# Optimization experiments

Measured on AMD Instinct MI355X. Metric: run time of the kernel, lower is better.

Reference implementation:

```python
import jax, jax.numpy as jnp
import numpy as np

B, S, I, H = 2, 400, 80, 128
F = 2 * H            # bidirectional feature dim
N = S + 1            # zero row prepended -> pairwise grid size
MAX_SEG = 50
NCLS = 50


def prelu(x, a):
    return jnp.where(x >= 0, x, a * x)


def lstm_dir(x, Wi, Wh, b, reverse=False):
    # x: (B, S, I); torch gate order: i, f, g, o
    if reverse:
        x = x[:, ::-1]
    Hd = Wh.shape[1]

    def step(carry, xt):
        h, c = carry
        gates = xt @ Wi.T + h @ Wh.T + b
        i_, f_, g_, o_ = jnp.split(gates, 4, axis=-1)
        c = jax.nn.sigmoid(f_) * c + jax.nn.sigmoid(i_) * jnp.tanh(g_)
        h = jax.nn.sigmoid(o_) * jnp.tanh(c)
        return (h, c), h

    h0 = jnp.zeros((x.shape[0], Hd), x.dtype)
    _, hs = jax.lax.scan(step, (h0, h0), jnp.swapaxes(x, 0, 1))
    hs = jnp.swapaxes(hs, 0, 1)
    if reverse:
        hs = hs[:, ::-1]
    return hs


def setup_inputs() -> dict:
    key = jax.random.key(0)
    ks = jax.random.split(key, 16)

    def rn(k, shape, s=0.05):
        return jax.random.normal(k, shape, jnp.float32) * s

    inp = {
        "x": jax.random.normal(ks[0], (B, S, I), jnp.float32),
        "lengths": jnp.full((B,), S, jnp.int32),
        "Wi_f": rn(ks[1], (4 * H, I)), "Wh_f": rn(ks[2], (4 * H, H)), "b_f": jnp.zeros((4 * H,), jnp.float32),
        "Wi_b": rn(ks[3], (4 * H, I)), "Wh_b": rn(ks[4], (4 * H, H)), "b_b": jnp.zeros((4 * H,), jnp.float32),
        "a1": jnp.full((1,), 0.25, jnp.float32),
        "W1": rn(ks[5], (100, 3 * F)), "b1": jnp.zeros((100,), jnp.float32),
        "a2": jnp.full((1,), 0.25, jnp.float32),
        "W2": rn(ks[6], (1, 100)), "b2": jnp.zeros((1,), jnp.float32),
        "ac1": jnp.full((1,), 0.25, jnp.float32),
        "Wc1": rn(ks[7], (2 * NCLS, F)), "bc1": jnp.zeros((2 * NCLS,), jnp.float32),
        "ac2": jnp.full((1,), 0.25, jnp.float32),
        "Wc2": rn(ks[8], (NCLS, 2 * NCLS)), "bc2": jnp.zeros((NCLS,), jnp.float32),
        "ab1": jnp.full((1,), 0.25, jnp.float32),
        "Wb1": rn(ks[9], (2 * NCLS, F)), "bb1": jnp.zeros((2 * NCLS,), jnp.float32),
        "ab2": jnp.full((1,), 0.25, jnp.float32),
        "Wb2": rn(ks[10], (2, 2 * NCLS)), "bb2": jnp.zeros((2,), jnp.float32),
    }
    return inp


def compute_scores(x, Wi_f, Wh_f, b_f, Wi_b, Wh_b, b_b, a1, W1, b1, a2, W2, b2):
    rnn_out = jnp.concatenate(
        [lstm_dir(x, Wi_f, Wh_f, b_f, False), lstm_dir(x, Wi_b, Wh_b, b_b, True)], axis=-1
    )  # (B, S, F)
    xp = jnp.concatenate([jnp.zeros((x.shape[0], 1, F), x.dtype), rnn_out], axis=1)  # (B, N, F)
    cum = jnp.cumsum(xp, axis=1)
    # phi[b,i,j] = concat(cum[j]-cum[i], xp[i], xp[j]); PReLU is elementwise with a
    # single shared parameter, and the first Linear is additive across the concat
    # blocks, so we decompose W1 instead of materializing the (B,N,N,3F) tensor.
    W1c, W1d, W1e = W1[:, :F], W1[:, F:2 * F], W1[:, 2 * F:]
    pc = prelu(cum[:, None, :, :] - cum[:, :, None, :], a1)  # (B, N, N, F)
    pxd = prelu(xp, a1) @ W1d.T                              # (B, N, 100)
    pxe = prelu(xp, a1) @ W1e.T                              # (B, N, 100)
    h = jnp.einsum('bijf,kf->bijk', pc, W1c) + pxd[:, :, None, :] + pxe[:, None, :, :] + b1
    scores = (prelu(h, a2) @ W2.T + b2)[..., 0]              # (B, N, N)
    return rnn_out, scores


def segment_search(scores):
    # DP: best[i] = max_{max(0,i-MAX_SEG) <= k < i} best[k] + scores[:, k, i]
    Bn, Nn = scores.shape[0], scores.shape[1]
    ks = jnp.arange(Nn)

    def dp_step(best, i):
        col = jnp.take(scores, i, axis=2)                    # (B, N)
        mask = (ks >= i - MAX_SEG) & (ks < i)
        cand = jnp.where(mask[None, :], best + col, -jnp.inf)
        m = cand.max(axis=1)
        k = cand.argmax(axis=1)
        best = best.at[:, i].set(m)
        return best, k

    best0 = jnp.zeros((Bn, Nn), scores.dtype)
    best, prev_tail = jax.lax.scan(dp_step, best0, jnp.arange(1, Nn))
    prev = jnp.concatenate([jnp.zeros((Bn, 1), jnp.int32),
                            prev_tail.T.astype(jnp.int32)], axis=1)  # (B, N)
    return best, prev


def reference(x, lengths, Wi_f, Wh_f, b_f, Wi_b, Wh_b, b_b, a1, W1, b1, a2, W2, b2,
              ac1, Wc1, bc1, ac2, Wc2, bc2, ab1, Wb1, bb1, ab2, Wb2, bb2):
    rnn_out, scores = compute_scores(x, Wi_f, Wh_f, b_f, Wi_b, Wh_b, b_b,
                                     a1, W1, b1, a2, W2, b2)
    cls_out = prelu(prelu(rnn_out, ac1) @ Wc1.T + bc1, ac2) @ Wc2.T + bc2
    bin_out = prelu(prelu(rnn_out, ab1) @ Wb1.T + bb1, ab2) @ Wb2.T + bb2
    best, prev = segment_search(scores)
    # pred score for the best segmentation ending at `lengths[b]` equals best[b, L]
    pred_scores = best[jnp.arange(scores.shape[0]), lengths]
    return scores, cls_out, bin_out, pred_scores, prev
```

## Files before the change

### kernel.cpp

```cpp
#include <hip/hip_runtime.h>
#include <hip/hip_fp16.h>
#include <math.h>

#define BB 2
#define SS 400
#define II 80
#define HH 128
#define FF 256
#define NN 401
#define G4 512
#define MAXSEG 50
#define NCLS 50
#define KH 100
#define KP 112
#define FRAGF 14336

#define SCORES_OFF 0
#define CLS_OFF    (BB*NN*NN)
#define BIN_OFF    (CLS_OFF + BB*SS*NCLS)
#define PRED_OFF   (BIN_OFF + BB*SS*2)
#define PREV_OFF   (PRED_OFF + BB)

#define WS_GX      0
#define WS_RNN     (WS_GX + 4*SS*G4)
#define WS_CUM     (WS_RNN + BB*SS*FF)
#define WS_PXD     (WS_CUM + BB*NN*FF)
#define WS_PXE     (WS_PXD + BB*NN*KP)
#define WS_PART    (WS_PXE + BB*NN*KP)
#define WS_W2P     (WS_PART + BB*16*FF)
#define WS_B1P     (WS_W2P + KP)
#define WS_WHP     (WS_B1P + KP)
#define WS_WFRAGC  (WS_WHP + 65536)
#define WS_WFRAGD  (WS_WFRAGC + FRAGF)
#define WS_WFRAGE  (WS_WFRAGD + FRAGF)
#define WS_WFRAGHC (WS_WFRAGE + FRAGF)
#define WS_WFRAGHB (WS_WFRAGHC + FRAGF)
#define WS_BC1P    (WS_WFRAGHB + FRAGF)
#define WS_BB1P    (WS_BC1P + KP)

typedef __attribute__((ext_vector_type(8))) short short8;
typedef __attribute__((ext_vector_type(4))) float f32x4;
typedef _Float16 f16x2 __attribute__((ext_vector_type(2)));
typedef _Float16 f16x8 __attribute__((ext_vector_type(8)));

__device__ __forceinline__ float prelu_f(float x, float a) {
    return x >= 0.f ? x : a * x;
}
__device__ __forceinline__ unsigned short f2bf(float x) {
    union { float f; unsigned u; } v; v.f = x;
    unsigned r = v.u + 0x7fffu + ((v.u >> 16) & 1u);
    return (unsigned short)(r >> 16);
}
__device__ __forceinline__ float fast_sigmoid(float x) {
    return 1.f / (1.f + __expf(-x));
}
__device__ __forceinline__ float fast_tanh(float x) {
    return 1.f - 2.f / (1.f + __expf(2.f * x));
}
__device__ __forceinline__ void barrier_lds() {
    asm volatile("s_waitcnt lgkmcnt(0)\ns_barrier" ::: "memory");
}
__device__ __forceinline__ void rec_barrier() {
    __builtin_amdgcn_sched_barrier(0);
    asm volatile("s_waitcnt lgkmcnt(0)");
    __builtin_amdgcn_s_barrier();
    __builtin_amdgcn_sched_barrier(0);
}
__device__ __forceinline__ int fragidx(int k, int f) {
    int kt = k >> 4, l15 = k & 15;
    int ks = f >> 5, quad = (f >> 3) & 3, e = f & 7;
    return ((((kt * 8 + ks) * 4 + quad) * 16) + l15) * 8 + e;
}

#define WPACKS (5 * KP)
#define PREPBLKS (WPACKS + G4)
__global__ void k_lstm_pre(const float* __restrict__ x,
                           const float* __restrict__ Wi_f, const float* __restrict__ b_f,
                           const float* __restrict__ Wi_b, const float* __restrict__ b_b,
                           float* __restrict__ gx,
                           const float* __restrict__ W1, const float* __restrict__ W2,
                           const float* __restrict__ b1,
                           const float* __restrict__ Wh_f, const float* __restrict__ Wh_b,
                           const float* __restrict__ Wc1, const float* __restrict__ Wb1,
                           const float* __restrict__ bc1, const float* __restrict__ bb1,
                           short* __restrict__ wfC, short* __restrict__ wfD,
                           short* __restrict__ wfE, short* __restrict__ wfHC,
                           short* __restrict__ wfHB,
                           float* __restrict__ w2p, float* __restrict__ b1p,
                           float* __restrict__ bc1p, float* __restrict__ bb1p,
                           __half* __restrict__ whp) {
    int blk0 = blockIdx.x;
    int tid = threadIdx.x;
    if (blk0 < WPACKS) {
        int which = blk0 / KP;
        int k = blk0 % KP;
        float w = 0.f;
        short* dst = wfC;
        if (which == 0)      { if (k < KH) w = W1[k * (3 * FF) + tid];          dst = wfC; }
        else if (which == 1) { if (k < KH) w = W1[k * (3 * FF) + FF + tid];     dst = wfD; }
        else if (which == 2) { if (k < KH) w = W1[k * (3 * FF) + 2 * FF + tid]; dst = wfE; }
        else if (which == 3) { if (k < KH) w = Wc1[k * FF + tid];               dst = wfHC; }
        else                 { if (k < KH) w = Wb1[k * FF + tid];               dst = wfHB; }
        dst[fragidx(k, tid)] = (short)f2bf(w);
        if (tid == 0) {
            if (which == 0) {
                w2p[k] = (k < KH) ? W2[k] : 0.f;
                b1p[k] = (k < KH) ? b1[k] : 0.f;
            } else if (which == 3) {
                bc1p[k] = (k < KH) ? bc1[k] : 0.f;
            } else if (which == 4) {
                bb1p[k] = (k < KH) ? bb1[k] : 0.f;
            }
        }
        return;
    }
    if (blk0 < PREPBLKS) {
        int gq = blk0 - WPACKS;
        int gate = gq >> 7;
        int unit = gq & 127;
        int wv = unit >> 4, col = unit & 15;
        int dir = tid >> 7, k = tid & 127;
        int kt = k >> 5, lanehi = (k >> 3) & 3, e = k & 7;
        int lane = lanehi * 16 + col;
        const float* Wh = dir ? Wh_b : Wh_f;
        whp[(size_t)(((((dir * 4 + gate) * 8 + wv) * 4 + kt) * 64) + lane) * 8 + e] =
            (__half)Wh[gq * HH + k];
        return;
    }
    int blk = blk0 - PREPBLKS;
    int t = blk % SS;
    int db = blk / SS;
    int b = db & 1, dir = db >> 1;
    const float* Wi = dir ? Wi_b : Wi_f;
    const float* bias = dir ? b_b : b_f;
    int xt = dir ? (SS - 1 - t) : t;

    __shared__ __align__(16) float xr[II];
    if (tid < II) xr[tid] = x[(b * SS + xt) * II + tid];
    __syncthreads();

    for (int g = tid; g < G4; g += 256) {
        const float* w = Wi + g * II;
        float acc = bias[g];
#pragma unroll
        for (int i = 0; i < II; i += 4) {
            float4 w4 = *(const float4*)(w + i);
            acc += w4.x * xr[i] + w4.y * xr[i + 1] + w4.z * xr[i + 2] + w4.w * xr[i + 3];
        }
        gx[((size_t)(db * SS + t) * HH + (g & 127)) * 4 + (g >> 7)] = acc;
    }
}

__global__ __launch_bounds__(512, 1)
void k_lstm_rec(const _Float16* __restrict__ whf, const float* __restrict__ gxr,
                float* __restrict__ rnn_out) {
    int db = blockIdx.x;
    int b = db & 1, dir = db >> 1;
    int tid = threadIdx.x;
    int wv = tid >> 6;
    int lane = tid & 63;

    f16x8 bf[4][4];
    {
        const f16x8* wp = (const f16x8*)whf;
#pragma unroll
        for (int g = 0; g < 4; ++g)
#pragma unroll
            for (int kt = 0; kt < 4; ++kt)
                bf[g][kt] = wp[((((dir * 4 + g) * 8 + wv) * 4 + kt) * 64) + lane];
    }

    __shared__ __align__(16) __half hsf[2][128];
    for (int i = tid; i < 256; i += 512) (&hsf[0][0])[i] = (__half)0.f;
    __syncthreads();

    float c_state = 0.f;
    const float4* gp4 = (const float4*)gxr + (size_t)(db * SS) * HH
                      + (wv << 4) + (lane & 15);

    float4 g0 = make_float4(0,0,0,0), g1 = g0, g2 = g0, g3 = g0;
    if (lane < 16) {
        g0 = gp4[0 * HH];
        g1 = gp4[1 * HH];
        g2 = gp4[2 * HH];
        g3 = gp4[3 * HH];
    }

    f16x8 a[4];
#pragma unroll
    for (int kt = 0; kt < 4; ++kt) a[kt] = (f16x8)(_Float16)0.f;

    int pb = 0;

#define REC_STEP(IOFF, G) do {                                                 \
        \
        if ((lane & 15) == 0) {                                                \
            _Pragma("unroll")                                                  \
            for (int kt = 0; kt < 4; ++kt)                                     \
                a[kt] = *(const f16x8*)(&hsf[pb][kt * 32 + (lane >> 4) * 8]);  \
        }                                                                      \
        f32x4 acc0 = (f32x4){0.f,0.f,0.f,0.f};                                 \
        f32x4 acc1 = acc0, acc2 = acc0, acc3 = acc0;                           \
        _Pragma("unroll")                                                      \
        for (int kt = 0; kt < 4; ++kt) {                                       \
            acc0 = __builtin_amdgcn_mfma_f32_16x16x32_f16(a[kt], bf[0][kt], acc0, 0, 0, 0); \
            acc1 = __builtin_amdgcn_mfma_f32_16x16x32_f16(a[kt], bf[1][kt], acc1, 0, 0, 0); \
            acc2 = __builtin_amdgcn_mfma_f32_16x16x32_f16(a[kt], bf[2][kt], acc2, 0, 0, 0); \
            acc3 = __builtin_amdgcn_mfma_f32_16x16x32_f16(a[kt], bf[3][kt], acc3, 0, 0, 0); \
        }                                                                      \
        if (lane < 16) {                                                       \
            float gi = acc0[0] + G.x;                                          \
            float gf = acc1[0] + G.y;                                          \
            float gg = acc2[0] + G.z;                                          \
            float go = acc3[0] + G.w;                                          \
            c_state = fast_sigmoid(gf) * c_state + fast_sigmoid(gi) * fast_tanh(gg); \
            float h = fast_sigmoid(go) * fast_tanh(c_state);                   \
            hsf[pb ^ 1][(wv << 4) + lane] = (__half)h;                         \
            int t_ = step + (IOFF);                                            \
            int xt = dir ? (SS - 1 - t_) : t_;                                 \
            rnn_out[(b * SS + xt) * FF + dir * HH + (wv << 4) + lane] = h;     \
                             \
            G = (t_ + 4 < SS) ? gp4[(size_t)(t_ + 4) * HH]                     \
                              : make_float4(0.f, 0.f, 0.f, 0.f);               \
        }                                                                      \
        rec_barrier();                                                         \
        pb ^= 1;                                                               \
    } while (0)

    for (int step = 0; step < SS; step += 4) {
        REC_STEP(0, g0);
        REC_STEP(1, g1);
        REC_STEP(2, g2);
        REC_STEP(3, g3);
    }
#undef REC_STEP
}

#define CHUNK 25
#define NCH 16
__global__ void k_cum_part(const float* __restrict__ rnn, float* __restrict__ part) {
    int blk = blockIdx.x;
    int c = blk % NCH, b = blk / NCH;
    int f = threadIdx.x;
    float s = 0.f;
    for (int r = 0; r < CHUNK; ++r) s += rnn[(b * SS + c * CHUNK + r) * FF + f];
    part[blk * FF + f] = s;
}
__global__ void k_cum_off(float* __restrict__ part) {
    int b = blockIdx.x;
    int f = threadIdx.x;
    float run = 0.f;
    for (int c = 0; c < NCH; ++c) {
        int idx = (b * NCH + c) * FF + f;
        float tmp = part[idx];
        part[idx] = run;
        run += tmp;
    }
}
__global__ void k_cum_write(const float* __restrict__ rnn, const float* __restrict__ part,
                            float* __restrict__ cum) {
    int blk = blockIdx.x;
    int c = blk % NCH, b = blk / NCH;
    int f = threadIdx.x;
    float run = part[blk * FF + f];
    cum[(b * NN + c * CHUNK) * FF + f] = run;
    for (int idx = 1; idx <= CHUNK; ++idx) {
        run += rnn[(b * SS + c * CHUNK + idx - 1) * FF + f];
        cum[(b * NN + c * CHUNK + idx) * FF + f] = run;
    }
}

#define PXBLKS 26
#define HDBLKS 25
#define AP 272
#define UCP 116
__global__ __launch_bounds__(256, 2)
void k_mlp(const float* __restrict__ rnn,
           const float* __restrict__ a1p,
           const float* __restrict__ ac1p, const float* __restrict__ ab1p,
           const short* __restrict__ wfD, const short* __restrict__ wfE,
           const short* __restrict__ wfHC, const short* __restrict__ wfHB,
           const float* __restrict__ bc1p, const float* __restrict__ bb1p,
           const float* __restrict__ ac2p, const float* __restrict__ ab2p,
           const float* __restrict__ Wc2, const float* __restrict__ bc2,
           const float* __restrict__ Wb2, const float* __restrict__ bb2,
           float* __restrict__ pxd, float* __restrict__ pxe,
           float* __restrict__ cls_out, float* __restrict__ bin_out) {
    int blk = blockIdx.x;
    int tid = threadIdx.x;
    bool is_px = (blk < PXBLKS);
    int rowbase = is_px ? blk * 32 : (blk - PXBLKS) * 32;
    int nrows_tot = is_px ? BB * NN : BB * SS;

    __shared__ __align__(16) short dth[2][32][AP];
    __shared__ float ucsh[2][32][UCP];

    {
        int row = tid >> 3;
        int fb = (tid & 7) * 32;
        int rg = rowbase + row;
        float src[32];
        if (is_px) {
            float a1 = a1p[0];
            int b = rg / NN, n = rg % NN;
            bool valid = (rg < nrows_tot) && (n > 0);
            const float* sp = valid ? (rnn + (b * SS + n - 1) * FF + fb) : nullptr;
#pragma unroll
            for (int c4 = 0; c4 < 8; ++c4) {
                float4 v = valid ? *(const float4*)(sp + c4 * 4) : make_float4(0,0,0,0);
                src[c4*4] = v.x; src[c4*4+1] = v.y; src[c4*4+2] = v.z; src[c4*4+3] = v.w;
            }
            union { short8 s; unsigned short u[8]; } h8;
#pragma unroll
            for (int c8 = 0; c8 < 4; ++c8) {
#pragma unroll
                for (int e = 0; e < 8; ++e) h8.u[e] = f2bf(prelu_f(src[c8*8+e], a1));
                *(short8*)(&dth[0][row][fb + c8 * 8]) = h8.s;
            }
        } else {
            float ac1 = ac1p[0], ab1 = ab1p[0];
            bool valid = (rg < nrows_tot);
            const float* sp = valid ? (rnn + rg * FF + fb) : nullptr;
#pragma unroll
            for (int c4 = 0; c4 < 8; ++c4) {
                float4 v = valid ? *(const float4*)(sp + c4 * 4) : make_float4(0,0,0,0);
                src[c4*4] = v.x; src[c4*4+1] = v.y; src[c4*4+2] = v.z; src[c4*4+3] = v.w;
            }
            union { short8 s; unsigned short u[8]; } hc, hb;
#pragma unroll
            for (int c8 = 0; c8 < 4; ++c8) {
#pragma unroll
                for (int e = 0; e < 8; ++e) {
                    hc.u[e] = f2bf(prelu_f(src[c8*8+e], ac1));
                    hb.u[e] = f2bf(prelu_f(src[c8*8+e], ab1));
                }
                *(short8*)(&dth[0][row][fb + c8 * 8]) = hc.s;
                *(short8*)(&dth[1][row][fb + c8 * 8]) = hb.s;
            }
        }
    }
    __syncthreads();

    int lane = tid & 63;
    int wv = tid >> 6;
    int quad = lane >> 4;
    int l15 = lane & 15;
    int kt0 = wv * 2, kt1 = wv * 2 + 1;
    bool has1 = (kt1 < 7);

    const short8* wp0 = (const short8*)(is_px ? wfD : wfHC);
    const short8* wp1 = (const short8*)(is_px ? wfE : wfHB);

    f32x4 acc[2][2][2];
#pragma unroll
    for (int p = 0; p < 2; ++p)
#pragma unroll
        for (int mt = 0; mt < 2; ++mt)
#pragma unroll
            for (int kk = 0; kk < 2; ++kk) acc[p][mt][kk] = (f32x4){0.f,0.f,0.f,0.f};

#pragma unroll
    for (int ks = 0; ks < 8; ++ks) {
        short8 b00 = wp0[((kt0 * 8 + ks) * 4 + quad) * 16 + l15];
        short8 b01 = has1 ? wp0[((kt1 * 8 + ks) * 4 + quad) * 16 + l15] : b00;
        short8 b10 = wp1[((kt0 * 8 + ks) * 4 + quad) * 16 + l15];
        short8 b11 = has1 ? wp1[((kt1 * 8 + ks) * 4 + quad) * 16 + l15] : b10;
#pragma unroll
        for (int mt = 0; mt < 2; ++mt) {
            short8 a0 = *(const short8*)(&dth[0][mt * 16 + l15][ks * 32 + quad * 8]);
            short8 a1v = is_px ? a0
                       : *(const short8*)(&dth[1][mt * 16 + l15][ks * 32 + quad * 8]);
            acc[0][mt][0] = __builtin_amdgcn_mfma_f32_16x16x32_bf16(a0, b00, acc[0][mt][0], 0, 0, 0);
            acc[1][mt][0] = __builtin_amdgcn_mfma_f32_16x16x32_bf16(a1v, b10, acc[1][mt][0], 0, 0, 0);
            if (has1) {
                acc[0][mt][1] = __builtin_amdgcn_mfma_f32_16x16x32_bf16(a0, b01, acc[0][mt][1], 0, 0, 0);
                acc[1][mt][1] = __builtin_amdgcn_mfma_f32_16x16x32_bf16(a1v, b11, acc[1][mt][1], 0, 0, 0);
            }
        }
    }

    int kout0 = kt0 * 16 + l15;
    int kout1 = has1 ? (kt1 * 16 + l15) : 0;

    if (is_px) {
#pragma unroll
        for (int mt = 0; mt < 2; ++mt) {
#pragma unroll
            for (int r = 0; r < 4; ++r) {
                int m = mt * 16 + quad * 4 + r;
                int rg = rowbase + m;
                if (rg < nrows_tot) {
                    pxd[rg * KP + kout0] = acc[0][mt][0][r];
                    pxe[rg * KP + kout0] = acc[1][mt][0][r];
                    if (has1) {
                        pxd[rg * KP + kout1] = acc[0][mt][1][r];
                        pxe[rg * KP + kout1] = acc[1][mt][1][r];
                    }
                }
            }
        }
        return;
    }

    float bc0 = bc1p[kout0], bc1v = bc1p[kout1];
    float bb0 = bb1p[kout0], bb1v = bb1p[kout1];
    float ac2 = ac2p[0], ab2 = ab2p[0];
#pragma unroll
    for (int mt = 0; mt < 2; ++mt) {
#pragma unroll
        for (int r = 0; r < 4; ++r) {
            int m = mt * 16 + quad * 4 + r;
            ucsh[0][m][kout0] = prelu_f(acc[0][mt][0][r] + bc0, ac2);
            ucsh[1][m][kout0] = prelu_f(acc[1][mt][0][r] + bb0, ab2);
            if (has1) {
                ucsh[0][m][kout1] = prelu_f(acc[0][mt][1][r] + bc1v, ac2);
                ucsh[1][m][kout1] = prelu_f(acc[1][mt][1][r] + bb1v, ab2);
            }
        }
    }
    __syncthreads();
    {
        int row = tid >> 3;
        int oc = tid & 7;
        int rg = rowbase + row;
        bool valid = (rg < nrows_tot);
        for (int o = oc; o < NCLS; o += 8) {
            float s = bc2[o];
            const float* w = Wc2 + o * KH;
#pragma unroll 4
            for (int k = 0; k < KH; ++k) s += w[k] * ucsh[0][row][k];
            if (valid) cls_out[rg * NCLS + o] = s;
        }
        if (tid < 64) {
            int row2 = tid >> 1, o = tid & 1;
            int rg2 = rowbase + row2;
            float s = bb2[o];
            const float* w = Wb2 + o * KH;
#pragma unroll 4
            for (int k = 0; k < KH; ++k) s += w[k] * ucsh[1][row2][k];
            if (rg2 < nrows_tot) bin_out[rg2 * 2 + o] = s;
        }
    }
}

#define JT 32
#define JTILES 13
#define NP2 201
__global__ __launch_bounds__(256, 3)
void k_scores(const float* __restrict__ cum,
              const short* __restrict__ wfrag,
              const float* __restrict__ pxd, const float* __restrict__ pxe,
              const float* __restrict__ b1p, const float* __restrict__ w2p,
              const float* __restrict__ b2p,
              const float* __restrict__ a1p, const float* __restrict__ a2p,
              float* __restrict__ scores, float* __restrict__ dpcol) {
    int blk = blockIdx.x;
    int jt = blk % JTILES;
    int ipair = (blk / JTILES) % NP2;
    int b = blk / (JTILES * NP2);
    int tid = threadIdx.x;
    float a1 = a1p[0], a2 = a2p[0];
    int jbase = jt * JT;
    int i0 = ipair * 2;
    int i1 = i0 + 1;
    bool has_i1 = (i1 <= SS);
    int i1c = has_i1 ? i1 : i0;

    __shared__ __align__(16) float cish[2][FF];
    __shared__ __align__(16) short dth[2][JT][AP];
    __shared__ float red[2][4][JT];

    cish[0][tid] = cum[(b * NN + i0) * FF + tid];
    cish[1][tid] = cum[(b * NN + i1c) * FF + tid];
    __syncthreads();

    {
        int row = tid >> 3;
        int fb = (tid & 7) * 32;
        int jg = jbase + row;
        int jc = (jg <= SS) ? jg : SS;
        const float* cj = cum + (b * NN + jc) * FF + fb;
        float4 v[8];
#pragma unroll
        for (int c8 = 0; c8 < 4; ++c8) {
            v[2 * c8] = *(const float4*)(cj + c8 * 8);
            v[2 * c8 + 1] = *(const float4*)(cj + c8 * 8 + 4);
        }
#pragma unroll
        for (int ii = 0; ii < 2; ++ii) {
            const float* cio = &cish[ii][0];
#pragma unroll
            for (int c8 = 0; c8 < 4; ++c8) {
                float dv[8] = { v[2*c8].x, v[2*c8].y, v[2*c8].z, v[2*c8].w,
                                v[2*c8+1].x, v[2*c8+1].y, v[2*c8+1].z, v[2*c8+1].w };
                union { short8 s; unsigned short u[8]; } h8;
#pragma unroll
                for (int e = 0; e < 8; ++e) {
                    float d = prelu_f(dv[e] - cio[fb + c8 * 8 + e], a1);
                    h8.u[e] = f2bf(d);
                }
                *(short8*)(&dth[ii][row][fb + c8 * 8]) = h8.s;
            }
        }
    }
    __syncthreads();

    int lane = tid & 63;
    int wv = tid >> 6;
    int quad = lane >> 4;
    int l15 = lane & 15;
    int kt0 = wv * 2, kt1 = wv * 2 + 1;
    bool has1 = (kt1 < 7);

    const short8* wf = (const short8*)wfrag;
    f32x4 acc[2][2][2];
#pragma unroll
    for (int ii = 0; ii < 2; ++ii)
#pragma unroll
        for (int mt = 0; mt < 2; ++mt)
#pragma unroll
            for (int kk = 0; kk < 2; ++kk) acc[ii][mt][kk] = (f32x4){0.f,0.f,0.f,0.f};

#pragma unroll
    for (int ks = 0; ks < 8; ++ks) {
        short8 b0 = wf[((kt0 * 8 + ks) * 4 + quad) * 16 + l15];
        short8 b1v = has1 ? wf[((kt1 * 8 + ks) * 4 + quad) * 16 + l15] : b0;
#pragma unroll
        for (int ii = 0; ii < 2; ++ii) {
#pragma unroll
            for (int mt = 0; mt < 2; ++mt) {
                short8 a = *(const short8*)(&dth[ii][mt * 16 + l15][ks * 32 + quad * 8]);
                acc[ii][mt][0] = __builtin_amdgcn_mfma_f32_16x16x32_bf16(a, b0, acc[ii][mt][0], 0, 0, 0);
                if (has1)
                    acc[ii][mt][1] = __builtin_amdgcn_mfma_f32_16x16x32_bf16(a, b1v, acc[ii][mt][1], 0, 0, 0);
            }
        }
    }

    int kout0 = kt0 * 16 + l15;
    int kout1 = has1 ? (kt1 * 16 + l15) : 0;
    float bb0 = b1p[kout0], bb1v = b1p[kout1];
    float w20 = w2p[kout0];
    float w21 = has1 ? w2p[kout1] : 0.f;

#pragma unroll
    for (int ii = 0; ii < 2; ++ii) {
        int iv = ii ? i1c : i0;
        float pd0 = pxd[(b * NN + iv) * KP + kout0];
        float pd1 = pxd[(b * NN + iv) * KP + kout1];
#pragma unroll
        for (int mt = 0; mt < 2; ++mt) {
#pragma unroll
            for (int r = 0; r < 4; ++r) {
                int m = mt * 16 + quad * 4 + r;
                int jg = jbase + m;
                int jc = (jg <= SS) ? jg : SS;
                float pe0 = pxe[(b * NN + jc) * KP + kout0];
                float pe1 = pxe[(b * NN + jc) * KP + kout1];
                float h0 = acc[ii][mt][0][r] + pd0 + pe0 + bb0;
                float s = w20 * prelu_f(h0, a2);
                float h1 = acc[ii][mt][1][r] + pd1 + pe1 + bb1v;
                s += w21 * prelu_f(h1, a2);
                s += __shfl_xor(s, 1);
                s += __shfl_xor(s, 2);
                s += __shfl_xor(s, 4);
                s += __shfl_xor(s, 8);
                if (l15 == 0) red[ii][wv][m] = s;
            }
        }
    }
    __syncthreads();
    if (tid < 2 * JT) {
        int ii = tid >> 5;
        int jl = tid & 31;
        int jg = jbase + jl;
        int iv = ii ? i1 : i0;
        if (jg <= SS && (ii == 0 || has_i1)) {
            float tot = red[ii][0][jl] + red[ii][1][jl] + red[ii][2][jl] + red[ii][3][jl] + b2p[0];
            scores[(b * NN + iv) * NN + jg] = tot;
            int d = jg - iv;
            if (d >= 1 && d <= MAXSEG) {
                dpcol[(b * NN + jg) * 64 + (iv & 63)] = tot;
            }
        }
    }
}

__global__ void k_dp(const float* __restrict__ dpcol, const int* __restrict__ lengths,
                     float* __restrict__ predF, float* __restrict__ prevF) {
    int b = blockIdx.x;
    int lane = threadIdx.x;
    int len = lengths[b];
    if (lane == 0) prevF[b * NN] = 0.f;

    float blr = 0.f;
    float predv = 0.f;

#define LO(I) (((I) > MAXSEG) ? ((I) - MAXSEG) : 0)
#define LOADCOL(ii) \
    ( ((ii) <= SS && (((lane - LO(ii)) & 63) < ((ii) - LO(ii)))) \
        ? dpcol[(b * NN + (ii)) * 64 + lane] : 0.f )

    float u0 = LOADCOL(1), u1 = LOADCOL(2), u2 = LOADCOL(3), u3 = LOADCOL(4);
    float u4 = LOADCOL(5), u5 = LOADCOL(6), u6 = LOADCOL(7), u7 = LOADCOL(8);

#define DPP_LVL(CTRL, v, k) do {                                              \
        int vo_i = __builtin_amdgcn_update_dpp(__float_as_int(v),             \
                       __float_as_int(v), (CTRL), 0xF, 0xF, false);           \
        int ko_  = __builtin_amdgcn_update_dpp((k), (k), (CTRL), 0xF, 0xF, false); \
        float vo = __int_as_float(vo_i);                                      \
        bool take = (vo > (v)) || (vo == (v) && ko_ < (k));                   \
        (v) = take ? vo : (v);                                                \
        (k) = take ? ko_ : (k);                                               \
    } while (0)

#define DP_STEP(I, BUF) do {                                                  \
        int lo_ = LO(I);                                                      \
        int cnt_ = (I) - lo_;                                                 \
        int off_ = (lane - lo_) & 63;                                         \
        float v_ = (off_ < cnt_) ? blr + BUF : -INFINITY;                     \
        int k_ = lo_ + off_;                                                  \
        DPP_LVL(0x111, v_, k_);                               \
        DPP_LVL(0x112, v_, k_);                               \
        DPP_LVL(0x114, v_, k_);                               \
        DPP_LVL(0x118, v_, k_);                               \
        DPP_LVL(0x142, v_, k_);                             \
        DPP_LVL(0x143, v_, k_);                             \
        int kb_ = __builtin_amdgcn_readlane(k_, 63);                          \
        float m_ = __int_as_float(                                            \
            __builtin_amdgcn_readlane(__float_as_int(v_), 63));               \
        if (lane == 0) {                                                      \
            prevF[b * NN + (I)] = (float)kb_;                                 \
            if ((I) == len) predv = m_;                                       \
        }                                                                     \
        if (lane == ((I) & 63)) blr = m_;                                     \
    } while (0)

    for (int i = 1; i <= SS; i += 8) {
        DP_STEP(i, u0);     u0 = LOADCOL(i + 8);
        DP_STEP(i + 1, u1); u1 = LOADCOL(i + 9);
        DP_STEP(i + 2, u2); u2 = LOADCOL(i + 10);
        DP_STEP(i + 3, u3); u3 = LOADCOL(i + 11);
        DP_STEP(i + 4, u4); u4 = LOADCOL(i + 12);
        DP_STEP(i + 5, u5); u5 = LOADCOL(i + 13);
        DP_STEP(i + 6, u6); u6 = LOADCOL(i + 14);
        DP_STEP(i + 7, u7); u7 = LOADCOL(i + 15);
    }
#undef DP_STEP
#undef DPP_LVL
#undef LOADCOL
#undef LO
    if (lane == 0) predF[b] = predv;
}

extern "C" void kernel_launch(void* const* d_in, const int* in_sizes, int n_in,
                              void* d_out, int out_size, void* d_ws, size_t ws_size,
                              hipStream_t stream) {
    const float* x    = (const float*)d_in[0];
    const int* lengths= (const int*)d_in[1];
    const float* Wi_f = (const float*)d_in[2];
    const float* Wh_f = (const float*)d_in[3];
    const float* b_f  = (const float*)d_in[4];
    const float* Wi_b = (const float*)d_in[5];
    const float* Wh_b = (const float*)d_in[6];
    const float* b_b  = (const float*)d_in[7];
    const float* a1   = (const float*)d_in[8];
    const float* W1   = (const float*)d_in[9];
    const float* b1   = (const float*)d_in[10];
    const float* a2   = (const float*)d_in[11];
    const float* W2   = (const float*)d_in[12];
    const float* b2   = (const float*)d_in[13];
    const float* ac1  = (const float*)d_in[14];
    const float* Wc1  = (const float*)d_in[15];
    const float* bc1  = (const float*)d_in[16];
    const float* ac2  = (const float*)d_in[17];
    const float* Wc2  = (const float*)d_in[18];
    const float* bc2  = (const float*)d_in[19];
    const float* ab1  = (const float*)d_in[20];
    const float* Wb1  = (const float*)d_in[21];
    const float* bb1  = (const float*)d_in[22];
    const float* ab2  = (const float*)d_in[23];
    const float* Wb2  = (const float*)d_in[24];
    const float* bb2  = (const float*)d_in[25];

    float* out = (float*)d_out;
    float* scores = out + SCORES_OFF;
    float* cls    = out + CLS_OFF;
    float* bin    = out + BIN_OFF;
    float* pred   = out + PRED_OFF;
    float* prev   = out + PREV_OFF;

    float* ws    = (float*)d_ws;
    float* gx    = ws + WS_GX;
    float* dpcol = ws + WS_GX;
    float* rnn   = ws + WS_RNN;
    float* cum   = ws + WS_CUM;
    float* pxd   = ws + WS_PXD;
    float* pxe   = ws + WS_PXE;
    float* part  = ws + WS_PART;
    float* w2p   = ws + WS_W2P;
    float* b1p   = ws + WS_B1P;
    __half* whp  = (__half*)(ws + WS_WHP);
    short* wfC   = (short*)(ws + WS_WFRAGC);
    short* wfD   = (short*)(ws + WS_WFRAGD);
    short* wfE   = (short*)(ws + WS_WFRAGE);
    short* wfHC  = (short*)(ws + WS_WFRAGHC);
    short* wfHB  = (short*)(ws + WS_WFRAGHB);
    float* bc1p  = ws + WS_BC1P;
    float* bb1p  = ws + WS_BB1P;

    k_lstm_pre<<<PREPBLKS + 4 * SS, 256, 0, stream>>>(x, Wi_f, b_f, Wi_b, b_b, gx,
                                                      W1, W2, b1, Wh_f, Wh_b,
                                                      Wc1, Wb1, bc1, bb1,
                                                      wfC, wfD, wfE, wfHC, wfHB,
                                                      w2p, b1p, bc1p, bb1p, whp);
    k_lstm_rec<<<4, 512, 0, stream>>>((const _Float16*)whp, gx, rnn);
    k_cum_part<<<BB * NCH, FF, 0, stream>>>(rnn, part);
    k_cum_off<<<BB, FF, 0, stream>>>(part);
    k_cum_write<<<BB * NCH, FF, 0, stream>>>(rnn, part, cum);
    k_mlp<<<PXBLKS + HDBLKS, 256, 0, stream>>>(rnn, a1, ac1, ab1,
                                               wfD, wfE, wfHC, wfHB,
                                               bc1p, bb1p, ac2, ab2,
                                               Wc2, bc2, Wb2, bb2,
                                               pxd, pxe, cls, bin);
    k_scores<<<BB * NP2 * JTILES, 256, 0, stream>>>(cum, wfC, pxd, pxe, b1p, w2p, b2,
                                                    a1, a2, scores, dpcol);
    k_dp<<<BB, 64, 0, stream>>>(dpcol, lengths, pred, prev);
}
```

Before: 638.1 us.

## Streamline LSTM recurrence step and merge prefix-sum kernels into one

The recurrent step now has every lane load the h fragments from shared memory directly, not just one lane per 16. The MFMA chain is fully unrolled with a zero-initialised first accumulate, and the gate prefetch uses a moving pointer with a peeled final iteration instead of per-step bounds checks. Output stores use an incrementing pointer rather than recomputed indices. The three-kernel chunked cumulative sum is replaced by one serial-scan kernel with 2 blocks, which saves two launches but serialises 400 rows per thread.

```diff
diff --git a/kernel.cpp b/kernel.cpp
--- a/kernel.cpp
+++ b/kernel.cpp
@@ -185,88 +185,77 @@
         g2 = gp4[2 * HH];
         g3 = gp4[3 * HH];
     }
-
-    f16x8 a[4];
-#pragma unroll
-    for (int kt = 0; kt < 4; ++kt) a[kt] = (f16x8)(_Float16)0.f;
-
+    const float4* gq = gp4 + (size_t)4 * HH;
+
+    float* outp = rnn_out + ((size_t)b * SS + (dir ? (SS - 1) : 0)) * FF
+                + dir * HH + (wv << 4) + lane;
+    const int ostep = dir ? -FF : FF;
+
+    const f32x4 z4 = (f32x4){0.f, 0.f, 0.f, 0.f};
     int pb = 0;
-
-#define REC_STEP(IOFF, G) do {                                                 \
-        \
-        if ((lane & 15) == 0) {                                                \
-            _Pragma("unroll")                                                  \
-            for (int kt = 0; kt < 4; ++kt)                                     \
-                a[kt] = *(const f16x8*)(&hsf[pb][kt * 32 + (lane >> 4) * 8]);  \
-        }                                                                      \
-        f32x4 acc0 = (f32x4){0.f,0.f,0.f,0.f};                                 \
-        f32x4 acc1 = acc0, acc2 = acc0, acc3 = acc0;                           \
-        _Pragma("unroll")                                                      \
-        for (int kt = 0; kt < 4; ++kt) {                                       \
-            acc0 = __builtin_amdgcn_mfma_f32_16x16x32_f16(a[kt], bf[0][kt], acc0, 0, 0, 0); \
-            acc1 = __builtin_amdgcn_mfma_f32_16x16x32_f16(a[kt], bf[1][kt], acc1, 0, 0, 0); \
-            acc2 = __builtin_amdgcn_mfma_f32_16x16x32_f16(a[kt], bf[2][kt], acc2, 0, 0, 0); \
-            acc3 = __builtin_amdgcn_mfma_f32_16x16x32_f16(a[kt], bf[3][kt], acc3, 0, 0, 0); \
-        }                                                                      \
+    int hib = (lane >> 4) * 8;
+
+#define REC_STEP(G, PF) do {                                                   \
+        f16x8 a0 = *(const f16x8*)(&hsf[pb][ 0 + hib]);                        \
+        f16x8 a1 = *(const f16x8*)(&hsf[pb][32 + hib]);                        \
+        f16x8 a2 = *(const f16x8*)(&hsf[pb][64 + hib]);                        \
+        f16x8 a3 = *(const f16x8*)(&hsf[pb][96 + hib]);                        \
+        f32x4 acc0 = __builtin_amdgcn_mfma_f32_16x16x32_f16(a0, bf[0][0], z4, 0, 0, 0); \
+        f32x4 acc1 = __builtin_amdgcn_mfma_f32_16x16x32_f16(a0, bf[1][0], z4, 0, 0, 0); \
+        f32x4 acc2 = __builtin_amdgcn_mfma_f32_16x16x32_f16(a0, bf[2][0], z4, 0, 0, 0); \
+        f32x4 acc3 = __builtin_amdgcn_mfma_f32_16x16x32_f16(a0, bf[3][0], z4, 0, 0, 0); \
+        acc0 = __builtin_amdgcn_mfma_f32_16x16x32_f16(a1, bf[0][1], acc0, 0, 0, 0); \
+        acc1 = __builtin_amdgcn_mfma_f32_16x16x32_f16(a1, bf[1][1], acc1, 0, 0, 0); \
+        acc2 = __builtin_amdgcn_mfma_f32_16x16x32_f16(a1, bf[2][1], acc2, 0, 0, 0); \
+        acc3 = __builtin_amdgcn_mfma_f32_16x16x32_f16(a1, bf[3][1], acc3, 0, 0, 0); \
+        acc0 = __builtin_amdgcn_mfma_f32_16x16x32_f16(a2, bf[0][2], acc0, 0, 0, 0); \
+        acc1 = __builtin_amdgcn_mfma_f32_16x16x32_f16(a2, bf[1][2], acc1, 0, 0, 0); \
+        acc2 = __builtin_amdgcn_mfma_f32_16x16x32_f16(a2, bf[2][2], acc2, 0, 0, 0); \
+        acc3 = __builtin_amdgcn_mfma_f32_16x16x32_f16(a2, bf[3][2], acc3, 0, 0, 0); \
+        acc0 = __builtin_amdgcn_mfma_f32_16x16x32_f16(a3, bf[0][3], acc0, 0, 0, 0); \
+        acc1 = __builtin_amdgcn_mfma_f32_16x16x32_f16(a3, bf[1][3], acc1, 0, 0, 0); \
+        acc2 = __builtin_amdgcn_mfma_f32_16x16x32_f16(a3, bf[2][3], acc2, 0, 0, 0); \
+        acc3 = __builtin_amdgcn_mfma_f32_16x16x32_f16(a3, bf[3][3], acc3, 0, 0, 0); \
         if (lane < 16) {                                                       \
             float gi = acc0[0] + G.x;                                          \
             float gf = acc1[0] + G.y;                                          \
             float gg = acc2[0] + G.z;                                          \
             float go = acc3[0] + G.w;                                          \
+            if (PF) { G = *gq; gq += HH; }         \
             c_state = fast_sigmoid(gf) * c_state + fast_sigmoid(gi) * fast_tanh(gg); \
             float h = fast_sigmoid(go) * fast_tanh(c_state);                   \
             hsf[pb ^ 1][(wv << 4) + lane] = (__half)h;                         \
-            int t_ = step + (IOFF);                                            \
-            int xt = dir ? (SS - 1 - t_) : t_;                                 \
-            rnn_out[(b * SS + xt) * FF + dir * HH + (wv << 4) + lane] = h;     \
-                             \
-            G = (t_ + 4 < SS) ? gp4[(size_t)(t_ + 4) * HH]                     \
-                              : make_float4(0.f, 0.f, 0.f, 0.f);               \
+            *outp = h;                                                         \
+            outp += ostep;                                                     \
         }                                                                      \
         rec_barrier();                                                         \
         pb ^= 1;                                                               \
     } while (0)
 
-    for (int step = 0; step < SS; step += 4) {
-        REC_STEP(0, g0);
-        REC_STEP(1, g1);
-        REC_STEP(2, g2);
-        REC_STEP(3, g3);
-    }
+    for (int it = 0; it < 99; ++it) {
+        REC_STEP(g0, 1);
+        REC_STEP(g1, 1);
+        REC_STEP(g2, 1);
+        REC_STEP(g3, 1);
+    }
+    REC_STEP(g0, 0);
+    REC_STEP(g1, 0);
+    REC_STEP(g2, 0);
+    REC_STEP(g3, 0);
 #undef REC_STEP
 }
 
-#define CHUNK 25
-#define NCH 16
-__global__ void k_cum_part(const float* __restrict__ rnn, float* __restrict__ part) {
-    int blk = blockIdx.x;
-    int c = blk % NCH, b = blk / NCH;
-    int f = threadIdx.x;
-    float s = 0.f;
-    for (int r = 0; r < CHUNK; ++r) s += rnn[(b * SS + c * CHUNK + r) * FF + f];
-    part[blk * FF + f] = s;
-}
-__global__ void k_cum_off(float* __restrict__ part) {
+__global__ void k_cum(const float* __restrict__ rnn, float* __restrict__ cum) {
     int b = blockIdx.x;
     int f = threadIdx.x;
     float run = 0.f;
-    for (int c = 0; c < NCH; ++c) {
-        int idx = (b * NCH + c) * FF + f;
-        float tmp = part[idx];
-        part[idx] = run;
-        run += tmp;
-    }
-}
-__global__ void k_cum_write(const float* __restrict__ rnn, const float* __restrict__ part,
-                            float* __restrict__ cum) {
-    int blk = blockIdx.x;
-    int c = blk % NCH, b = blk / NCH;
-    int f = threadIdx.x;
-    float run = part[blk * FF + f];
-    cum[(b * NN + c * CHUNK) * FF + f] = run;
-    for (int idx = 1; idx <= CHUNK; ++idx) {
-        run += rnn[(b * SS + c * CHUNK + idx - 1) * FF + f];
-        cum[(b * NN + c * CHUNK + idx) * FF + f] = run;
+    cum[(size_t)(b * NN) * FF + f] = 0.f;
+    const float* rp = rnn + (size_t)b * SS * FF + f;
+    float* cp = cum + ((size_t)b * NN + 1) * FF + f;
+#pragma unroll 8
+    for (int t = 0; t < SS; ++t) {
+        run += rp[(size_t)t * FF];
+        cp[(size_t)t * FF] = run;
     }
 }
 
@@ -697,7 +686,6 @@
     float* cum   = ws + WS_CUM;
     float* pxd   = ws + WS_PXD;
     float* pxe   = ws + WS_PXE;
-    float* part  = ws + WS_PART;
     float* w2p   = ws + WS_W2P;
     float* b1p   = ws + WS_B1P;
     __half* whp  = (__half*)(ws + WS_WHP);
@@ -715,9 +703,7 @@
                                                       wfC, wfD, wfE, wfHC, wfHB,
                                                       w2p, b1p, bc1p, bb1p, whp);
     k_lstm_rec<<<4, 512, 0, stream>>>((const _Float16*)whp, gx, rnn);
-    k_cum_part<<<BB * NCH, FF, 0, stream>>>(rnn, part);
-    k_cum_off<<<BB, FF, 0, stream>>>(part);
-    k_cum_write<<<BB * NCH, FF, 0, stream>>>(rnn, part, cum);
+    k_cum<<<BB, FF, 0, stream>>>(rnn, cum);
     k_mlp<<<PXBLKS + HDBLKS, 256, 0, stream>>>(rnn, a1, ac1, ab1,
                                                wfD, wfE, wfHC, wfHB,
                                                bc1p, bb1p, ac2, ab2,
```

Result: no change. 648.7 us (+1.7%).
